# Kernel tuning notes

Hardware: AMD Instinct MI355X
Metric: run time of the kernel (lower is better)

The kernel has to match this reference:

```python
import jax, jax.numpy as jnp
import numpy as np

V = 27578   # super-model vertex count (self.shape)
NJ = 24     # joints
NB = 10     # shape PCA coeffs
NP = (NJ - 1) * 9  # 207 pose-blend features
K = 24000   # kept vertices (to_keep)
B = 32
# standard SMPL kinematic tree: PARENTS[i] is the parent joint of joint i (i>=1)
PARENTS = np.array([0, 0, 0, 0, 1, 2, 3, 4, 5, 6, 7, 8, 9, 9, 9, 12, 13, 14, 16, 17, 18, 19, 20, 21], dtype=np.int32)


def setup_inputs() -> dict:
    key = jax.random.key(0)
    ks = jax.random.split(key, 8)
    pose = jax.random.normal(ks[0], (B, NJ, 3), dtype=jnp.float32) * 0.4
    betas = jax.random.normal(ks[1], (B, NB + 1), dtype=jnp.float32)  # last entry = gender flag
    J_regressor = jax.random.uniform(ks[2], (2, NJ, V), dtype=jnp.float32)
    J_regressor = J_regressor / jnp.sum(J_regressor, axis=-1, keepdims=True)
    v_template = jax.random.normal(ks[3], (2, V, 3), dtype=jnp.float32)
    shapedirs = jax.random.normal(ks[4], (2, V, 3, NB), dtype=jnp.float32) * 0.03
    posedirs = jax.random.normal(ks[5], (2, V, 3, NP), dtype=jnp.float32) * 0.01
    weights_all = jax.random.uniform(ks[6], (2, V, NJ), dtype=jnp.float32)
    weights_all = weights_all / jnp.sum(weights_all, axis=-1, keepdims=True)
    to_keep = jnp.sort(jax.random.randint(ks[7], (K,), 0, V, dtype=jnp.int32))
    return {"pose": pose, "betas": betas, "J_regressor": J_regressor,
            "v_template": v_template, "shapedirs": shapedirs, "posedirs": posedirs,
            "weights_all": weights_all, "to_keep": to_keep}


def rodrigues(r):
    """Axis-angle [N,3] -> rotation matrices [N,3,3] (Rodrigues formula)."""
    eps = jnp.float32(np.finfo(np.float32).eps)
    theta = jnp.maximum(jnp.linalg.norm(r, axis=-1, keepdims=True), eps)  # [N,1]
    rh = r / theta
    z = jnp.zeros_like(rh[:, 0])
    m = jnp.stack([z, -rh[:, 2], rh[:, 1],
                   rh[:, 2], z, -rh[:, 0],
                   -rh[:, 1], rh[:, 0], z], axis=1).reshape(-1, 3, 3)
    t = theta[:, :, None]  # [N,1,1]
    I = jnp.eye(3, dtype=r.dtype)
    return I + m * jnp.sin(t) + jnp.matmul(m, m) * (1.0 - jnp.cos(t))


def reference(pose, betas, J_regressor, v_template, shapedirs, posedirs, weights_all, to_keep):
    b = betas.shape[0]
    dt = pose.dtype
    g = betas[:, -1] > 0.5  # gender: True -> male (index 1)
    sel = lambda f, m: jnp.where(g[:, None, None], m, f)

    # shape blendshapes for both genders, select per sample
    vs_f = jnp.einsum('bs,vcs->bvc', betas[:, :NB], shapedirs[0]) + v_template[0]
    vs_m = jnp.einsum('bs,vcs->bvc', betas[:, :NB], shapedirs[1]) + v_template[1]

    J_f = jnp.einsum('jv,bvc->bjc', J_regressor[0], vs_f)
    J_m = jnp.einsum('jv,bvc->bjc', J_regressor[1], vs_m)
    J = sel(J_f, J_m)  # [b,24,3]

    # Rodrigues per joint
    R = rodrigues(pose.reshape(-1, 3)).reshape(b, NJ, 3, 3)

    # pose blendshapes
    lrot = (R[:, 1:] - jnp.eye(3, dtype=dt)).reshape(b, NP)  # [b,207]
    off_f = jnp.einsum('bp,vcp->bvc', lrot, posedirs[0])
    off_m = jnp.einsum('bp,vcp->bvc', lrot, posedirs[1])
    v_posed = sel(vs_f, vs_m) + sel(off_f, off_m)  # [b,V,3]

    # local joint transforms [b,24,4,4]
    J_rel = jnp.concatenate([J[:, :1], J[:, 1:] - J[:, PARENTS[1:]]], axis=1)
    A = jnp.concatenate([R, J_rel[..., None]], axis=-1)  # [b,24,3,4]
    bottom = jnp.broadcast_to(jnp.array([0., 0., 0., 1.], dtype=dt), (b, NJ, 1, 4))
    A = jnp.concatenate([A, bottom], axis=2)

    # kinematic chain (sequential 24-joint tree)
    Gs = [A[:, 0]]
    for i in range(1, NJ):
        Gs.append(jnp.matmul(Gs[int(PARENTS[i])], A[:, i]))
    G = jnp.stack(Gs, axis=1)  # [b,24,4,4]

    # subtract rest-pose joint contribution: results = G - pack(G @ [J;0])
    Jh0 = jnp.concatenate([J, jnp.zeros((b, NJ, 1), dtype=dt)], axis=-1)
    corr = jnp.einsum('bjpq,bjq->bjp', G, Jh0)
    results = G.at[:, :, :, 3].add(-corr)

    Jh1 = jnp.concatenate([J, jnp.ones((b, NJ, 1), dtype=dt)], axis=-1)
    joints = jnp.einsum('bjpq,bjq->bjp', results, Jh1)[:, :, :3]

    # linear blend skinning with gender-matched weights
    w = jnp.where(g[:, None, None], weights_all[1][None], weights_all[0][None])  # [b,V,24]
    T = jnp.einsum('bjpq,bvj->bvpq', results, w)  # [b,V,4,4]
    vh = jnp.concatenate([v_posed, jnp.ones((b, V, 1), dtype=dt)], axis=-1)
    v = jnp.einsum('bvpq,bvq->bvp', T, vh)[:, :, :3]

    root = joints[:, :1]
    result = (v - root)[:, to_keep, :]  # [b,K,3]
    return result
```

## Files before the change

### kernel.cpp

```cpp
#include <hip/hip_runtime.h>
#include <hip/hip_bf16.h>
#include <cstdint>
#include <cstddef>

#define V      27578
#define NJ     24
#define KK     24000
#define NT2    1724
#define NCHUNK 25
#define VCHUNK 1104

#define LPD    0
#define LA     12288
#define LRB    16000
#define LVP    24192
#define LT     26368
#define LWA    36608
#define LTM2   37120
#define LROOT2 37216
#define LPERM2 37312
#define LCNT2  37344
#define LKB    37348
#define LDSW   37364

#define WS_JS   0
#define WS_LA   39600
#define WS_RB   43312
#define WS_ROOT 51824
#define WS_PERM 51920
#define WS_CNT  51952
#define WS_KB   51956

typedef short short8 __attribute__((ext_vector_type(8)));
typedef float f32x4 __attribute__((ext_vector_type(4)));
typedef float f32x4a __attribute__((ext_vector_type(4), aligned(4)));

union S8U4 { unsigned u[4]; uint4 u4; short8 s; };

__device__ __forceinline__ unsigned pk2(float a, float b) {
    __hip_bfloat162 h = __float22bfloat162_rn(float2{a, b});
    union { __hip_bfloat162 h; unsigned u; } cv; cv.h = h;
    return cv.u;
}

__constant__ int d_par[24] = {0,0,0,0,1,2,3,4,5,6,7,8,9,9,9,12,13,14,16,17,18,19,20,21};

__global__ __launch_bounds__(256) void k_js(const float* __restrict__ jreg,
                                            const float* __restrict__ vtmpl,
                                            const float* __restrict__ sdirs,
                                            float* __restrict__ ws) {
    const int chunk = blockIdx.x, jg = blockIdx.y, g = blockIdx.z;
    const int tid = threadIdx.x;
    float acc[4][33];
#pragma unroll
    for (int a = 0; a < 4; ++a)
#pragma unroll
        for (int o = 0; o < 33; ++o) acc[a][o] = 0.f;

    const int v0 = chunk * VCHUNK;
    const int v1 = (v0 + VCHUNK < V) ? v0 + VCHUNK : V;
    const float* jr0 = jreg + (size_t)g * NJ * V;
    const float* sd  = sdirs + (size_t)g * V * 30;
    const float* tm  = vtmpl + (size_t)g * V * 3;

    for (int v = v0 + tid; v < v1; v += 256) {
        float jv[4];
#pragma unroll
        for (int a = 0; a < 4; ++a) jv[a] = jr0[(size_t)(jg*4 + a) * V + v];
        float b[33];
        const float* sdv = sd + (size_t)v * 30;
#pragma unroll
        for (int o = 0; o < 30; o += 2) {
            float2 q = *(const float2*)(sdv + o);
            b[o] = q.x; b[o+1] = q.y;
        }
        b[30] = tm[(size_t)v*3 + 0];
        b[31] = tm[(size_t)v*3 + 1];
        b[32] = tm[(size_t)v*3 + 2];
#pragma unroll
        for (int a = 0; a < 4; ++a)
#pragma unroll
            for (int o = 0; o < 33; ++o) acc[a][o] += jv[a] * b[o];
    }

#pragma unroll
    for (int a = 0; a < 4; ++a)
#pragma unroll
        for (int o = 0; o < 33; ++o) {
            float x = acc[a][o];
#pragma unroll
            for (int s = 32; s >= 1; s >>= 1) x += __shfl_xor(x, s, 64);
            acc[a][o] = x;
        }

    __shared__ float red[4][132];
    const int wvi = tid >> 6, ln = tid & 63;
    if (ln == 0) {
#pragma unroll
        for (int a = 0; a < 4; ++a)
#pragma unroll
            for (int o = 0; o < 33; ++o) red[wvi][a*33 + o] = acc[a][o];
    }
    __syncthreads();
    if (tid < 132) {
        float s = red[0][tid] + red[1][tid] + red[2][tid] + red[3][tid];
        int a = tid / 33, o = tid % 33;
        int j = jg * 4 + a;
        ws[(size_t)((g*NJ + j)*33 + o) * NCHUNK + chunk] = s;
    }
}

__global__ __launch_bounds__(256) void k_joint(const float* __restrict__ pose,
                                               const float* __restrict__ betas,
                                               const int*   __restrict__ to_keep,
                                               float* __restrict__ ws) {
    const int bid = (int)blockIdx.x;
    const int t = threadIdx.x;
    int* wsI = (int*)ws;
    unsigned* wsU = (unsigned*)ws;

    if (bid >= 32) {
        int idx = (bid - 32) * 256 + t;
        if (idx <= NT2) {
            int target = idx * 16;
            int lo = 0, hi = KK;
            while (lo < hi) { int m = (lo + hi) >> 1; if (to_keep[m] < target) lo = m + 1; else hi = m; }
            wsI[WS_KB + idx] = lo;
        }
        return;
    }

    __shared__ float gflag[32];
    __shared__ int   permJ[33];
    __shared__ float jsJ[792];
    __shared__ float Jloc[96];
    __shared__ float AJ[288];
    __shared__ float GS[288];

    if (t < 32) gflag[t] = betas[t*11 + 10];
    __syncthreads();
    if (t < 32) {
        bool male = gflag[t] > 0.5f;
        unsigned gm = (unsigned)__ballot(male);
        int cnt0 = 32 - __popc(gm);
        unsigned below = (1u << t) - 1u;
        int slot = male ? (cnt0 + __popc(gm & below)) : __popc((~gm) & below);
        permJ[slot] = t;
        if (t == 0) permJ[32] = cnt0;
    }
    __syncthreads();

    const int slot = bid;
    const int b = permJ[slot];
    const int gi = (gflag[b] > 0.5f) ? 1 : 0;

    if (bid == 0) {
        if (t < 32) wsI[WS_PERM + t] = permJ[t];
        if (t == 0) wsI[WS_CNT] = permJ[32];
    }

    for (int o = t; o < 792; o += 256) {
        const float* p = ws + WS_JS + (size_t)(gi*792 + o) * NCHUNK;
        float s = 0.f;
#pragma unroll
        for (int c = 0; c < NCHUNK; ++c) s += p[c];
        jsJ[o] = s;
    }
    __syncthreads();

    if (t < 72) {
        int j = t / 3, c = t - 3*j;
        const float* jsb = jsJ + j*33;
        float s = jsb[30 + c];
#pragma unroll
        for (int q = 0; q < 10; ++q) s += jsb[c*10 + q] * betas[b*11 + q];
        Jloc[j*4 + c] = s;
    }
    __syncthreads();

    if (t < 24) {
        const float* pp = pose + (size_t)(b*24 + t) * 3;
        float rx = pp[0], ry = pp[1], rz = pp[2];
        float th = fmaxf(sqrtf(rx*rx + ry*ry + rz*rz), 1.1920929e-07f);
        float inv = 1.0f / th;
        float ux = rx*inv, uy = ry*inv, uz = rz*inv;
        float st = sinf(th), ct = cosf(th), oc = 1.0f - ct;
        float* A = AJ + t*12;
        A[0] = ct + oc*ux*ux;    A[1] = oc*ux*uy - st*uz; A[2]  = oc*ux*uz + st*uy;
        A[4] = oc*ux*uy + st*uz; A[5] = ct + oc*uy*uy;    A[6]  = oc*uy*uz - st*ux;
        A[8] = oc*ux*uz - st*uy; A[9] = oc*uy*uz + st*ux; A[10] = ct + oc*uz*uz;
        int par = d_par[t];
#pragma unroll
        for (int r = 0; r < 3; ++r)
            A[r*4 + 3] = Jloc[t*4 + r] - (t > 0 ? Jloc[par*4 + r] : 0.f);
    }
    __syncthreads();

    if (t < 116) {
        float f[2];
#pragma unroll
        for (int h = 0; h < 2; ++h) {
            int k = 2*t + h;
            float val = 0.f;
            if (k < 207) {
                int j = k / 9 + 1, rc = k - 9*(j-1);
                int r = rc / 3, c = rc - 3*r;
                val = AJ[j*12 + r*4 + c] - (r == c ? 1.f : 0.f);
            } else if (k >= 208 && k < 218) {
                val = betas[b*11 + (k - 208)];
            }
            f[h] = val;
        }
        wsU[WS_LA + slot*116 + t] = pk2(f[0], f[1]);
    }

    if (t < 12) {
        constexpr int kPar[24] = {0,0,0,0,1,2,3,4,5,6,7,8,9,9,9,12,13,14,16,17,18,19,20,21};
        const int r = t >> 2, c = t & 3;
        float Greg[24];
        Greg[0] = AJ[t];
#pragma unroll
        for (int j = 1; j < 24; ++j) {
            const int par = kPar[j];
            float a0 = AJ[j*12 + 0 + c];
            float a1 = AJ[j*12 + 4 + c];
            float a2 = AJ[j*12 + 8 + c];
            float g0 = __shfl(Greg[par], r*4 + 0, 64);
            float g1 = __shfl(Greg[par], r*4 + 1, 64);
            float g2 = __shfl(Greg[par], r*4 + 2, 64);
            float g3 = __shfl(Greg[par], r*4 + 3, 64);
            Greg[j] = g0*a0 + g1*a1 + g2*a2 + (c == 3 ? g3 : 0.f);
        }
#pragma unroll
        for (int j = 0; j < 24; ++j) {
            float t0 = __shfl(Greg[j], r*4 + 0, 64);
            float t1 = __shfl(Greg[j], r*4 + 1, 64);
            float t2 = __shfl(Greg[j], r*4 + 2, 64);
            float corr = t0*Jloc[j*4 + 0] + t1*Jloc[j*4 + 1] + t2*Jloc[j*4 + 2];
            if (c == 3) Greg[j] -= corr;
            GS[j*12 + t] = Greg[j];
        }
    }
    __syncthreads();

    {
        int kg = t >> 6, rem = t & 63, n = rem >> 2, wq = rem & 3;
        int j0 = kg*8 + 2*wq;
        float f0 = (j0 < 24 && n < 12) ? GS[j0*12 + n] : 0.f;
        float f1 = (j0 + 1 < 24 && n < 12) ? GS[(j0+1)*12 + n] : 0.f;
        wsU[WS_RB + slot*256 + t] = pk2(f0, f1);
    }
    if (t < 3) {
        float s = GS[t*4 + 3];
#pragma unroll
        for (int q = 0; q < 3; ++q) s += GS[t*4 + q] * Jloc[q];
        ws[WS_ROOT + slot*3 + t] = s;
    }
}

__global__ __launch_bounds__(1024) void k_pose(const float* __restrict__ posedirs,
                                               const float* __restrict__ sdirs,
                                               const float* __restrict__ vtmpl,
                                               const float* __restrict__ wall,
                                               const int*   __restrict__ to_keep,
                                               const float* __restrict__ ws,
                                               float* __restrict__ out) {
    extern __shared__ float L[];
    unsigned* Lu = (unsigned*)L;
    int* Li = (int*)L;
    const unsigned* wsU = (const unsigned*)ws;
    const int* wsI = (const int*)ws;
    const int t = threadIdx.x;
    const int l = t & 63, wv = t >> 6;
    const int lm = l & 15, lg = l >> 4;
    const int bid = (int)blockIdx.x;

    int pdoff[5], pdladr[5];
    bool pdok[5], pdq3[5];
#pragma unroll
    for (int n = 0; n < 5; ++n) {
        int e = t + 1024*n;
        bool ok = e < 4992;
        pdok[n] = ok;
        int e2 = ok ? e : 0;
        int row = e2 / 52, k4 = (e2 - 52*row) * 4;
        int g = row / 48, rr = row - 48*g;
        pdoff[n] = g*(V*621) + rr*207 + k4;
        int kw = k4 >> 1;
        pdladr[n] = LPD + row*128 + (kw ^ ((row & 7) << 2));
        pdq3[n] = (k4 == 204);
    }
    int sdoff = 0, sdladr = 0;
    if (t < 480) {
        int w = 2*t;
        int g = w / 480, w2 = w - 480*g;
        int row = w2 / 10, j = (w2 - 10*row) >> 1;
        int rowg = g*48 + row;
        sdoff = g*(V*30) + w2;
        sdladr = LPD + rowg*128 + ((104 + j) ^ ((rowg & 7) << 2));
    }
    int tmoff = 0;
    if (t < 48)  { int w = 2*t; int g = w/48;  tmoff = g*(V*3) + (w - 48*g); }
    int woff = 0, wladr = 0;
    if (t < 384) {
        int g = t/192, i = t - 192*g;
        int v = i/12, wi = i - 12*v;
        int kgrp = wi >> 2, wq = wi & 3;
        int j0 = kgrp*8 + 2*wq;
        woff = g*(V*24) + v*24 + j0;
        wladr = LWA + g*256 + kgrp*64 + v*4 + wq;
    }

    float4 pdreg[5]; float2 sdreg = {0,0}, tmreg = {0,0}, wreg = {0,0};

    const int PDLIM = 2*V*621 - 4;
    const int SDLIM = 2*V*30 - 2;
    const int TMLIM = 2*V*3 - 2;
    const int WLIM  = 2*V*24 - 2;

    auto issue_loads = [&](int itm) {
        const int vb = itm * 16;
#pragma unroll
        for (int n = 0; n < 5; ++n) {
            int a = vb*621 + pdoff[n];
            if (a > PDLIM) a = PDLIM;
            f32x4a q = *(const f32x4a*)(posedirs + a);
            pdreg[n].x = q.x;
            pdreg[n].y = q.y;
            pdreg[n].z = q.z;
            pdreg[n].w = pdq3[n] ? 0.f : q.w;
        }
        const int vb2 = itm * 16;
        if (t < 480) { int a = vb2*30 + sdoff; if (a > SDLIM) a = SDLIM; sdreg = *(const float2*)(sdirs + a); }
        if (t < 48)  { int a = vb2*3  + tmoff; if (a > TMLIM) a = TMLIM; tmreg = *(const float2*)(vtmpl + a); }
        if (t < 384) { int a = vb2*24 + woff;  if (a > WLIM)  a = WLIM;  wreg  = *(const float2*)(wall  + a); }
    };

    auto write_stage = [&]() {
#pragma unroll
        for (int n = 0; n < 5; ++n)
            if (pdok[n]) {
                uint2 v;
                v.x = pk2(pdreg[n].x, pdreg[n].y);
                v.y = pk2(pdreg[n].z, pdreg[n].w);
                *(uint2*)&Lu[pdladr[n]] = v;
            }
        if (t < 480) Lu[sdladr] = pk2(sdreg.x, sdreg.y);
        if (t < 48)  { L[LTM2 + 2*t] = tmreg.x; L[LTM2 + 2*t + 1] = tmreg.y; }
        if (t < 384) Lu[wladr] = pk2(wreg.x, wreg.y);
    };

    issue_loads(bid);

    {
        for (int i = t; i < 928; i += 1024)
            *(uint4*)&Lu[LA + 4*i] = *(const uint4*)&wsU[WS_LA + 4*i];
        for (int i = t; i < 2048; i += 1024)
            *(uint4*)&Lu[LRB + 4*i] = *(const uint4*)&wsU[WS_RB + 4*i];
        if (t < 96)  L[LROOT2 + t] = ws[WS_ROOT + t];
        if (t < 32)  Li[LPERM2 + t] = wsI[WS_PERM + t];
        if (t == 0)  Li[LCNT2] = wsI[WS_CNT];
        if (t < 8) {
            int idx = bid + 256*t;
            int kst = KK, ken = KK;
            if (idx < NT2) { kst = wsI[WS_KB + idx]; ken = wsI[WS_KB + idx + 1]; }
            Li[LKB + t] = kst; Li[LKB + 8 + t] = ken;
        }
        if (t < 128) Lu[LWA + (t >> 6)*256 + 192 + (t & 63)] = 0;
        if (t < 288) {
            int row = t / 3, j2 = 109 + (t - 3*(t/3));
            Lu[LPD + row*128 + (j2 ^ ((row & 7) << 2))] = 0;
        }
        __syncthreads();
    }

    const int cnt0v = Li[LCNT2];
    const int cnt1 = 32 - cnt0v;
    const int m0 = (cnt0v + 15) >> 4, m1 = (cnt1 + 15) >> 4;
    const int ntA = 3*m0, ntasks = 3*(m0 + m1);

    int rb0 = -1, nt0 = 0, sb0 = 0, ct0 = 0, gi0 = 0;
    if (wv < ntasks) {
        int gi = (wv >= ntA) ? 1 : 0; int tt = gi ? wv - ntA : wv;
        int mt = tt / 3; nt0 = tt - 3*mt;
        sb0 = gi ? cnt0v : 0; ct0 = gi ? cnt1 : cnt0v;
        rb0 = sb0 + mt*16; gi0 = gi;
    }

    const int bs = t >> 5, kl0 = t & 31;
    const int borig = Li[LPERM2 + bs];
    const float rt0 = L[LROOT2 + bs*3 + 0];
    const float rt1 = L[LROOT2 + bs*3 + 1];
    const float rt2 = L[LROOT2 + bs*3 + 2];
    const int s4 = (lm & 7) << 2;

    write_stage();
    __syncthreads();

    int li = 0;
    for (int item = bid; item < NT2; item += 256, ++li) {
        const bool more = (item + 256 < NT2);
        if (more) issue_loads(item + 256);

        f32x4 acc0 = {0,0,0,0};
        if (rb0 >= 0) {
            const unsigned* ap = Lu + LA + (rb0 + lm)*116 + (lg << 2);
            const unsigned* bp = Lu + LPD + (gi0*48 + nt0*16 + lm)*128;
#pragma unroll
            for (int kk = 0; kk < 7; ++kk) {
                S8U4 a; a.u4 = *(const uint4*)(ap + kk*16);
                S8U4 bb; bb.u4 = *(const uint4*)(bp + ((kk*16 + (lg << 2)) ^ s4));
                acc0 = __builtin_amdgcn_mfma_f32_16x16x32_bf16(a.s, bb.s, acc0, 0, 0, 0);
            }
        }

        if (rb0 >= 0) {
            int n = nt0*16 + lm;
            int vd = n / 3, cd = n - 3*vd;
            float tmv = L[LTM2 + gi0*48 + n];
#pragma unroll
            for (int r = 0; r < 4; ++r) {
                int slot = rb0 + (lg << 2) + r;
                if ((unsigned)(slot - sb0) < (unsigned)ct0)
                    L[LVP + slot*68 + vd*4 + cd] = acc0[r] + tmv;
            }
        }

#pragma unroll
        for (int q = 0; q < 2; ++q) {
            int s = wv*2 + q;
            int gsl = (s >= cnt0v) ? 1 : 0;
            S8U4 a; a.u4 = *(const uint4*)(Lu + LWA + gsl*256 + lg*64 + lm*4);
            S8U4 b; b.u4 = *(const uint4*)(Lu + LRB + s*256 + lg*64 + lm*4);
            f32x4 acT = {0,0,0,0};
            acT = __builtin_amdgcn_mfma_f32_16x16x32_bf16(a.s, b.s, acT, 0, 0, 0);
#pragma unroll
            for (int r = 0; r < 4; ++r)
                L[LT + s*320 + (lg*4 + r)*20 + lm] = acT[r];
        }
        __syncthreads();

        const int kst = Li[LKB + li], ken = Li[LKB + 8 + li];
        const int v0w = item * 16;
        for (int k = kst + kl0; k < ken; k += 32) {
            const int vr = to_keep[k] - v0w;
            const float4 vp = *(const float4*)&L[LVP + bs*68 + vr*4];
            const float4 t0 = *(const float4*)&L[LT + bs*320 + vr*20];
            const float4 t1 = *(const float4*)&L[LT + bs*320 + vr*20 + 4];
            const float4 t2 = *(const float4*)&L[LT + bs*320 + vr*20 + 8];
            const size_t ob = ((size_t)borig*KK + (size_t)k)*3;
            out[ob]   = t0.x*vp.x + t0.y*vp.y + t0.z*vp.z + t0.w - rt0;
            out[ob+1] = t1.x*vp.x + t1.y*vp.y + t1.z*vp.z + t1.w - rt1;
            out[ob+2] = t2.x*vp.x + t2.y*vp.y + t2.z*vp.z + t2.w - rt2;
        }
        if (more) write_stage();
        __syncthreads();
    }
}

extern "C" void kernel_launch(void* const* d_in, const int* in_sizes, int n_in,
                              void* d_out, int out_size, void* d_ws, size_t ws_size,
                              hipStream_t stream) {
    const float* pose     = (const float*)d_in[0];
    const float* betas    = (const float*)d_in[1];
    const float* jreg     = (const float*)d_in[2];
    const float* vtmpl    = (const float*)d_in[3];
    const float* sdirs    = (const float*)d_in[4];
    const float* posedirs = (const float*)d_in[5];
    const float* wall     = (const float*)d_in[6];
    const int*   to_keep  = (const int*)d_in[7];
    float* ws  = (float*)d_ws;
    float* out = (float*)d_out;

    hipFuncSetAttribute((const void*)k_pose,
                        hipFuncAttributeMaxDynamicSharedMemorySize,
                        LDSW * 4);

    hipLaunchKernelGGL(k_js,    dim3(NCHUNK, 6, 2), dim3(256), 0, stream, jreg, vtmpl, sdirs, ws);
    hipLaunchKernelGGL(k_joint, dim3(40),           dim3(256), 0, stream, pose, betas, to_keep, ws);
    hipLaunchKernelGGL(k_pose,  dim3(256),          dim3(1024), LDSW * 4, stream,
                       posedirs, sdirs, vtmpl, wall, to_keep, ws, out);
}
```

Baseline: 79.98 us.

## Split batch across two block halves and fuse skinning into MFMA epilogue

Result: slower. 142.2 us (+77.8%).

```diff
diff --git a/kernel.cpp b/kernel.cpp
--- a/kernel.cpp
+++ b/kernel.cpp
@@ -12,16 +12,16 @@
 
 #define LPD    0
 #define LA     12288
-#define LRB    16000
-#define LVP    24192
-#define LT     26368
-#define LWA    36608
-#define LTM2   37120
-#define LROOT2 37216
-#define LPERM2 37312
-#define LCNT2  37344
-#define LKB    37348
-#define LDSW   37364
+#define LRB    14144
+#define LVP    18240
+#define LWA    19328
+#define LTM2   19840
+#define LROOT2 19936
+#define LPERM2 20032
+#define LCNT2  20064
+#define LKB    20068
+#define LKVS   20084
+#define LDSW   20104
 
 #define WS_JS   0
 #define WS_LA   39600
@@ -258,13 +258,13 @@
     }
 }
 
-__global__ __launch_bounds__(1024) void k_pose(const float* __restrict__ posedirs,
-                                               const float* __restrict__ sdirs,
-                                               const float* __restrict__ vtmpl,
-                                               const float* __restrict__ wall,
-                                               const int*   __restrict__ to_keep,
-                                               const float* __restrict__ ws,
-                                               float* __restrict__ out) {
+__global__ __launch_bounds__(1024, 8) void k_pose(const float* __restrict__ posedirs,
+                                                  const float* __restrict__ sdirs,
+                                                  const float* __restrict__ vtmpl,
+                                                  const float* __restrict__ wall,
+                                                  const int*   __restrict__ to_keep,
+                                                  const float* __restrict__ ws,
+                                                  float* __restrict__ out) {
     extern __shared__ float L[];
     unsigned* Lu = (unsigned*)L;
     int* Li = (int*)L;
@@ -274,6 +274,9 @@
     const int l = t & 63, wv = t >> 6;
     const int lm = l & 15, lg = l >> 4;
     const int bid = (int)blockIdx.x;
+    const int h = bid >> 8;
+    const int ib = bid & 255;
+    const int hbase = h << 4;
 
     int pdoff[5], pdladr[5];
     bool pdok[5], pdq3[5];
@@ -330,10 +333,9 @@
             pdreg[n].z = q.z;
             pdreg[n].w = pdq3[n] ? 0.f : q.w;
         }
-        const int vb2 = itm * 16;
-        if (t < 480) { int a = vb2*30 + sdoff; if (a > SDLIM) a = SDLIM; sdreg = *(const float2*)(sdirs + a); }
-        if (t < 48)  { int a = vb2*3  + tmoff; if (a > TMLIM) a = TMLIM; tmreg = *(const float2*)(vtmpl + a); }
-        if (t < 384) { int a = vb2*24 + woff;  if (a > WLIM)  a = WLIM;  wreg  = *(const float2*)(wall  + a); }
+        if (t < 480) { int a = vb*30 + sdoff; if (a > SDLIM) a = SDLIM; sdreg = *(const float2*)(sdirs + a); }
+        if (t < 48)  { int a = vb*3  + tmoff; if (a > TMLIM) a = TMLIM; tmreg = *(const float2*)(vtmpl + a); }
+        if (t < 384) { int a = vb*24 + woff;  if (a > WLIM)  a = WLIM;  wreg  = *(const float2*)(wall  + a); }
     };
 
     auto write_stage = [&]() {
@@ -350,18 +352,17 @@
         if (t < 384) Lu[wladr] = pk2(wreg.x, wreg.y);
     };
 
-    issue_loads(bid);
+    issue_loads(ib);
 
     {
-        for (int i = t; i < 928; i += 1024)
-            *(uint4*)&Lu[LA + 4*i] = *(const uint4*)&wsU[WS_LA + 4*i];
-        for (int i = t; i < 2048; i += 1024)
-            *(uint4*)&Lu[LRB + 4*i] = *(const uint4*)&wsU[WS_RB + 4*i];
+        if (t < 464)
+            *(uint4*)&Lu[LA + 4*t] = *(const uint4*)&wsU[WS_LA + h*1856 + 4*t];
+        *(uint4*)&Lu[LRB + 4*t] = *(const uint4*)&wsU[WS_RB + h*4096 + 4*t];
         if (t < 96)  L[LROOT2 + t] = ws[WS_ROOT + t];
         if (t < 32)  Li[LPERM2 + t] = wsI[WS_PERM + t];
         if (t == 0)  Li[LCNT2] = wsI[WS_CNT];
         if (t < 8) {
-            int idx = bid + 256*t;
+            int idx = ib + 256*t;
             int kst = KK, ken = KK;
             if (idx < NT2) { kst = wsI[WS_KB + idx]; ken = wsI[WS_KB + idx + 1]; }
             Li[LKB + t] = kst; Li[LKB + 8 + t] = ken;
@@ -376,35 +377,54 @@
 
     const int cnt0v = Li[LCNT2];
     const int cnt1 = 32 - cnt0v;
-    const int m0 = (cnt0v + 15) >> 4, m1 = (cnt1 + 15) >> 4;
-    const int ntA = 3*m0, ntasks = 3*(m0 + m1);
-
-    int rb0 = -1, nt0 = 0, sb0 = 0, ct0 = 0, gi0 = 0;
-    if (wv < ntasks) {
-        int gi = (wv >= ntA) ? 1 : 0; int tt = gi ? wv - ntA : wv;
-        int mt = tt / 3; nt0 = tt - 3*mt;
-        sb0 = gi ? cnt0v : 0; ct0 = gi ? cnt1 : cnt0v;
-        rb0 = sb0 + mt*16; gi0 = gi;
-    }
-
-    const int bs = t >> 5, kl0 = t & 31;
-    const int borig = Li[LPERM2 + bs];
-    const float rt0 = L[LROOT2 + bs*3 + 0];
-    const float rt1 = L[LROOT2 + bs*3 + 1];
-    const float rt2 = L[LROOT2 + bs*3 + 2];
+
+    int rb0 = -1, nt0 = 0, gi0 = 0, wlo = 0, whi = 0;
+    {
+        int tcount = 0;
+#pragma unroll
+        for (int gi = 0; gi < 2; ++gi) {
+            int gs = gi ? cnt0v : 0, gc = gi ? cnt1 : cnt0v;
+            int mtiles = (gc + 15) >> 4;
+#pragma unroll
+            for (int mt = 0; mt < 2; ++mt) {
+                if (mt >= mtiles) continue;
+                int base = gs + mt*16;
+                int lo = base > hbase ? base : hbase;
+                int hi = base + 16 < gs + gc ? base + 16 : gs + gc;
+                if (hi > hbase + 16) hi = hbase + 16;
+                if (lo >= hi) continue;
+                if (wv >= tcount && wv < tcount + 3) {
+                    rb0 = base; nt0 = wv - tcount; gi0 = gi; wlo = lo; whi = hi;
+                }
+                tcount += 3;
+            }
+        }
+    }
+
+    const int sg = hbase + wv;
+    const int borig = Li[LPERM2 + sg];
+    const int gslw = (sg >= cnt0v) ? 1 : 0;
     const int s4 = (lm & 7) << 2;
 
     write_stage();
     __syncthreads();
 
     int li = 0;
-    for (int item = bid; item < NT2; item += 256, ++li) {
+    for (int item = ib; item < NT2; item += 256, ++li) {
         const bool more = (item + 256 < NT2);
         if (more) issue_loads(item + 256);
 
+        if (t >= 1007) {
+            int vv = t - 1007;
+            int lo = Li[LKB + li], hi = Li[LKB + 8 + li];
+            int target = item*16 + vv;
+            while (lo < hi) { int m = (lo + hi) >> 1; if (to_keep[m] < target) lo = m + 1; else hi = m; }
+            Li[LKVS + vv] = lo;
+        }
+
         f32x4 acc0 = {0,0,0,0};
         if (rb0 >= 0) {
-            const unsigned* ap = Lu + LA + (rb0 + lm)*116 + (lg << 2);
+            const unsigned* ap = Lu + LA + (rb0 - hbase + lm)*116 + (lg << 2);
             const unsigned* bp = Lu + LPD + (gi0*48 + nt0*16 + lm)*128;
 #pragma unroll
             for (int kk = 0; kk < 7; ++kk) {
@@ -421,37 +441,42 @@
 #pragma unroll
             for (int r = 0; r < 4; ++r) {
                 int slot = rb0 + (lg << 2) + r;
-                if ((unsigned)(slot - sb0) < (unsigned)ct0)
-                    L[LVP + slot*68 + vd*4 + cd] = acc0[r] + tmv;
-            }
-        }
-
-#pragma unroll
-        for (int q = 0; q < 2; ++q) {
-            int s = wv*2 + q;
-            int gsl = (s >= cnt0v) ? 1 : 0;
-            S8U4 a; a.u4 = *(const uint4*)(Lu + LWA + gsl*256 + lg*64 + lm*4);
-            S8U4 b; b.u4 = *(const uint4*)(Lu + LRB + s*256 + lg*64 + lm*4);
-            f32x4 acT = {0,0,0,0};
+                if (slot >= wlo && slot < whi)
+                    L[LVP + (slot - hbase)*68 + vd*4 + cd] = acc0[r] + tmv;
+            }
+        }
+
+        f32x4 acT = {0,0,0,0};
+        {
+            S8U4 a; a.u4 = *(const uint4*)(Lu + LWA + gslw*256 + lg*64 + lm*4);
+            S8U4 b; b.u4 = *(const uint4*)(Lu + LRB + wv*256 + lg*64 + lm*4);
             acT = __builtin_amdgcn_mfma_f32_16x16x32_bf16(a.s, b.s, acT, 0, 0, 0);
-#pragma unroll
-            for (int r = 0; r < 4; ++r)
-                L[LT + s*320 + (lg*4 + r)*20 + lm] = acT[r];
         }
         __syncthreads();
 
-        const int kst = Li[LKB + li], ken = Li[LKB + 8 + li];
-        const int v0w = item * 16;
-        for (int k = kst + kl0; k < ken; k += 32) {
-            const int vr = to_keep[k] - v0w;
-            const float4 vp = *(const float4*)&L[LVP + bs*68 + vr*4];
-            const float4 t0 = *(const float4*)&L[LT + bs*320 + vr*20];
-            const float4 t1 = *(const float4*)&L[LT + bs*320 + vr*20 + 4];
-            const float4 t2 = *(const float4*)&L[LT + bs*320 + vr*20 + 8];
-            const size_t ob = ((size_t)borig*KK + (size_t)k)*3;
-            out[ob]   = t0.x*vp.x + t0.y*vp.y + t0.z*vp.z + t0.w - rt0;
-            out[ob+1] = t1.x*vp.x + t1.y*vp.y + t1.z*vp.z + t1.w - rt1;
-            out[ob+2] = t2.x*vp.x + t2.y*vp.y + t2.z*vp.z + t2.w - rt2;
+        {
+            float term[4];
+#pragma unroll
+            for (int r = 0; r < 4; ++r) {
+                int q = lm & 3;
+                float m = (q < 3) ? L[LVP + wv*68 + ((lg << 2) + r)*4 + q] : 1.0f;
+                float x = acT[r] * m;
+                x += __shfl_xor(x, 1, 64);
+                x += __shfl_xor(x, 2, 64);
+                term[r] = x;
+            }
+            if ((lm & 3) == 0 && lm < 12) {
+                int p = lm >> 2;
+                float rt = L[LROOT2 + sg*3 + p];
+#pragma unroll
+                for (int r = 0; r < 4; ++r) {
+                    int v = (lg << 2) + r;
+                    int k0 = Li[LKVS + v], k1 = Li[LKVS + v + 1];
+                    float val = term[r] - rt;
+                    for (int k = k0; k < k1; ++k)
+                        out[((size_t)borig*KK + (size_t)k)*3 + p] = val;
+                }
+            }
         }
         if (more) write_stage();
         __syncthreads();
@@ -478,6 +503,6 @@
 
     hipLaunchKernelGGL(k_js,    dim3(NCHUNK, 6, 2), dim3(256), 0, stream, jreg, vtmpl, sdirs, ws);
     hipLaunchKernelGGL(k_joint, dim3(40),           dim3(256), 0, stream, pose, betas, to_keep, ws);
-    hipLaunchKernelGGL(k_pose,  dim3(256),          dim3(1024), LDSW * 4, stream,
+    hipLaunchKernelGGL(k_pose,  dim3(512),          dim3(1024), LDSW * 4, stream,
                        posedirs, sdirs, vtmpl, wall, to_keep, ws, out);
 }
```
